# Optimization experiments

Hardware: AMD Instinct MI355X
Metric: run time of the kernel (lower is better)

The kernel has to match this reference:

```python
import jax, jax.numpy as jnp
import numpy as np

N_EMBD = 1024
N_HEAD = 16
HEAD_DIM = N_EMBD // N_HEAD
B, T = 2, 2048
EPS = 1e-5


def _layernorm(x, gamma, beta):
    mu = jnp.mean(x, axis=-1, keepdims=True)
    var = jnp.mean((x - mu) ** 2, axis=-1, keepdims=True)
    return gamma * (x - mu) / jnp.sqrt(var + EPS) + beta


def setup_inputs() -> dict:
    key = jax.random.key(0)
    ks = jax.random.split(key, 12)
    s = 0.02
    d, f = N_EMBD, 4 * N_EMBD
    return {
        "x": jax.random.normal(ks[0], (B, T, d), dtype=jnp.float32),
        "ln1_g": jnp.ones((d,), jnp.float32),
        "ln1_b": jnp.zeros((d,), jnp.float32),
        "wq": jax.random.normal(ks[1], (d, d), jnp.float32) * s,
        "bq": jnp.zeros((d,), jnp.float32),
        "wk": jax.random.normal(ks[2], (d, d), jnp.float32) * s,
        "bk": jnp.zeros((d,), jnp.float32),
        "wv": jax.random.normal(ks[3], (d, d), jnp.float32) * s,
        "bv": jnp.zeros((d,), jnp.float32),
        "wo": jax.random.normal(ks[4], (d, d), jnp.float32) * s,
        "bo": jnp.zeros((d,), jnp.float32),
        "ln2_g": jnp.ones((d,), jnp.float32),
        "ln2_b": jnp.zeros((d,), jnp.float32),
        "w1": jax.random.normal(ks[5], (d, f), jnp.float32) * s,
        "b1": jnp.zeros((f,), jnp.float32),
        "w2": jax.random.normal(ks[6], (f, d), jnp.float32) * s,
        "b2": jnp.zeros((d,), jnp.float32),
    }


def reference(x, ln1_g, ln1_b, wq, bq, wk, bk, wv, bv, wo, bo,
              ln2_g, ln2_b, w1, b1, w2, b2):
    Bn, Tn, C = x.shape
    # --- attention branch (dropout = identity, eval mode) ---
    xn = _layernorm(x, ln1_g, ln1_b)
    q = (xn @ wq + bq).reshape(Bn, Tn, N_HEAD, HEAD_DIM)
    k = (xn @ wk + bk).reshape(Bn, Tn, N_HEAD, HEAD_DIM)
    v = (xn @ wv + bv).reshape(Bn, Tn, N_HEAD, HEAD_DIM)
    scale = 1.0 / jnp.sqrt(jnp.float32(HEAD_DIM))
    scores = jnp.einsum("bqhd,bkhd->bhqk", q, k) * scale  # [B,H,T,T]
    causal = jnp.tril(jnp.ones((Tn, Tn), dtype=bool))
    scores = jnp.where(causal[None, None], scores, -jnp.inf)
    weights = jax.nn.softmax(scores, axis=-1)
    attn = jnp.einsum("bhqk,bkhd->bqhd", weights, v).reshape(Bn, Tn, C)
    x = x + (attn @ wo + bo)
    # --- MLP branch ---
    h = _layernorm(x, ln2_g, ln2_b)
    h = jax.nn.gelu(h @ w1 + b1, approximate=False)
    x = x + (h @ w2 + b2)
    return x
```

## Files before the change

kernel.cpp:

```cpp
#include <hip/hip_runtime.h>
#include <stdint.h>

#define T_SEQ 2048
#define NHEAD 16
#define HDIM 64
#define CDIM 1024
#define FDIM 4096
#define MROWS 4096
#define NQB 32

typedef __bf16 bf16;
typedef __bf16 bf16x8 __attribute__((ext_vector_type(8)));
typedef float f32x4 __attribute__((ext_vector_type(4)));

__device__ __forceinline__ void gload_lds16(const void* g, void* l) {
  __builtin_amdgcn_global_load_lds(
      (const __attribute__((address_space(1))) void*)g,
      (__attribute__((address_space(3))) void*)l, 16, 0, 0);
}

__device__ __forceinline__ void wt_body(const float* __restrict__ src,
                                        bf16* __restrict__ dst, int K, int N,
                                        int k0, int n0) {
  __shared__ float tile[64][65];
  int tid = threadIdx.x;
  int r4 = tid >> 4, c4 = (tid & 15) * 4;
#pragma unroll
  for (int p = 0; p < 4; ++p) {
    int r = p * 16 + r4;
    float4 v = *(const float4*)&src[(size_t)(k0 + r) * N + n0 + c4];
    tile[r][c4] = v.x; tile[r][c4 + 1] = v.y;
    tile[r][c4 + 2] = v.z; tile[r][c4 + 3] = v.w;
  }
  __syncthreads();
  int n8 = tid >> 3, k8 = (tid & 7) * 8;
#pragma unroll
  for (int p = 0; p < 2; ++p) {
    int n = p * 32 + n8;
    union { bf16 h[8]; uint4 u; } t;
#pragma unroll
    for (int j = 0; j < 8; ++j) t.h[j] = (bf16)tile[k8 + j][n];
    *(uint4*)&dst[(size_t)(n0 + n) * K + k0 + k8] = t.u;
  }
}

__global__ void wt_kernel(const float* __restrict__ src, bf16* __restrict__ dst,
                          int K, int N) {
  wt_body(src, dst, K, N, blockIdx.y * 64, blockIdx.x * 64);
}

__global__ void wt4_kernel(const float* s0, const float* s1, const float* s2,
                           const float* s3, bf16* d0, bf16* d1, bf16* d2, bf16* d3) {
  const float* src = blockIdx.z == 0 ? s0 : blockIdx.z == 1 ? s1 : blockIdx.z == 2 ? s2 : s3;
  bf16* dst = blockIdx.z == 0 ? d0 : blockIdx.z == 1 ? d1 : blockIdx.z == 2 ? d2 : d3;
  wt_body(src, dst, 1024, 1024, blockIdx.y * 64, blockIdx.x * 64);
}

__global__ void vt_kernel(const bf16* __restrict__ v, bf16* __restrict__ vt) {
  __shared__ bf16 tile[64][65];
  int bh = blockIdx.y;
  int t0 = blockIdx.x * 64;
  int tid = threadIdx.x;
  const bf16* src = v + (size_t)bh * T_SEQ * HDIM;
  bf16* dst = vt + (size_t)bh * HDIM * T_SEQ;
  int r8 = tid >> 3, c8 = (tid & 7) * 8;
#pragma unroll
  for (int p = 0; p < 2; ++p) {
    int r = p * 32 + r8;
    union { uint4 u; bf16 h[8]; } t;
    t.u = *(const uint4*)&src[(size_t)(t0 + r) * HDIM + c8];
#pragma unroll
    for (int j = 0; j < 8; ++j) tile[r][c8 + j] = t.h[j];
  }
  __syncthreads();
#pragma unroll
  for (int p = 0; p < 2; ++p) {
    int d = p * 32 + r8;
    union { uint4 u; bf16 h[8]; } t;
#pragma unroll
    for (int j = 0; j < 8; ++j) t.h[j] = tile[c8 + j][d];
    *(uint4*)&dst[(size_t)d * T_SEQ + t0 + c8] = t.u;
  }
}

__global__ __launch_bounds__(256)
void ln_kernel(const float* __restrict__ x, const float* __restrict__ g,
               const float* __restrict__ b, bf16* __restrict__ out) {
  int row = blockIdx.x;
  int tid = threadIdx.x;
  float4 v = *(const float4*)&x[(size_t)row * CDIM + tid * 4];
  float s = v.x + v.y + v.z + v.w;
  float ss = v.x * v.x + v.y * v.y + v.z * v.z + v.w * v.w;
#pragma unroll
  for (int off = 1; off < 64; off <<= 1) {
    s += __shfl_xor(s, off, 64);
    ss += __shfl_xor(ss, off, 64);
  }
  __shared__ float red[8];
  int wv = tid >> 6, ln = tid & 63;
  if (ln == 0) { red[wv] = s; red[4 + wv] = ss; }
  __syncthreads();
  s = red[0] + red[1] + red[2] + red[3];
  ss = red[4] + red[5] + red[6] + red[7];
  float mu = s * (1.0f / CDIM);
  float var = ss * (1.0f / CDIM) - mu * mu;
  float rstd = rsqrtf(var + 1e-5f);
  float4 gv = *(const float4*)&g[tid * 4];
  float4 bv = *(const float4*)&b[tid * 4];
  union { bf16 h[4]; uint2 u; } o;
  o.h[0] = (bf16)(gv.x * (v.x - mu) * rstd + bv.x);
  o.h[1] = (bf16)(gv.y * (v.y - mu) * rstd + bv.y);
  o.h[2] = (bf16)(gv.z * (v.z - mu) * rstd + bv.z);
  o.h[3] = (bf16)(gv.w * (v.w - mu) * rstd + bv.w);
  *(uint2*)&out[(size_t)row * CDIM + tid * 4] = o.u;
}

enum { EPI_QKV = 0, EPI_F32RES = 1, EPI_GELU = 2 };

template <int EPI, int TN>
__global__ __launch_bounds__(256, 2)
void gemm_bt(const bf16* __restrict__ A, const bf16* __restrict__ Bt,
             const float* __restrict__ bias, const float* __restrict__ bias2,
             const float* __restrict__ bias3, const float* res,
             void* outp, void* out2, void* out3, int M, int N, int K) {
  constexpr int MR = (TN == 128) ? 4 : 2;
  __shared__ __align__(16) bf16 As[4][128 * 32];
  __shared__ __align__(16) bf16 Bs[4][TN * 32];
  int tid = threadIdx.x;
  int w = tid >> 6, l = tid & 63;
  int lo = l & 15, g = l >> 4;
  int rowb = (TN == 128) ? (w >> 1) * 64 : w * 32;
  int colb = (TN == 128) ? (w & 1) * 64 : 0;

  int nwg = gridDim.x * gridDim.y;
  int orig = blockIdx.y * gridDim.x + blockIdx.x;
  int lid = (orig & 7) * (nwg >> 3) + (orig >> 3);
  int bx = lid % gridDim.x, by = lid / gridDim.x;
  int m0 = by * 128, n0 = bx * TN;

  f32x4 acc[MR][4];
#pragma unroll
  for (int i = 0; i < MR; ++i)
#pragma unroll
    for (int j = 0; j < 4; ++j) acc[i][j] = (f32x4){0.f, 0.f, 0.f, 0.f};

  const bf16* Ab = A + (size_t)m0 * K;
  const bf16* Bb = Bt + (size_t)n0 * K;

  auto STAGE = [&](int t, int buf) {
    int k0 = t * 32;
    int row = (l >> 2);
    int col = ((l & 3) ^ ((l >> 3) & 3)) * 8;
#pragma unroll
    for (int i = 0; i < 2; ++i) {
      int c = w * 2 + i;
      gload_lds16(Ab + (size_t)(c * 16 + row) * K + k0 + col, &As[buf][c * 512]);
    }
    if constexpr (TN == 128) {
#pragma unroll
      for (int i = 0; i < 2; ++i) {
        int c = w * 2 + i;
        gload_lds16(Bb + (size_t)(c * 16 + row) * K + k0 + col, &Bs[buf][c * 512]);
      }
    } else {
      int c = w;
      gload_lds16(Bb + (size_t)(c * 16 + row) * K + k0 + col, &Bs[buf][c * 512]);
    }
  };

  int nt = K >> 5;
  STAGE(0, 0);
  STAGE(1, 1);
  STAGE(2, 2);
  int sw = (lo >> 1) & 3;
  for (int t = 0; t < nt; ++t) {
    if constexpr (TN == 128) {
      if (t + 2 < nt)      asm volatile("s_waitcnt vmcnt(8)" ::: "memory");
      else if (t + 1 < nt) asm volatile("s_waitcnt vmcnt(4)" ::: "memory");
      else                 asm volatile("s_waitcnt vmcnt(0)" ::: "memory");
    } else {
      if (t + 2 < nt)      asm volatile("s_waitcnt vmcnt(6)" ::: "memory");
      else if (t + 1 < nt) asm volatile("s_waitcnt vmcnt(3)" ::: "memory");
      else                 asm volatile("s_waitcnt vmcnt(0)" ::: "memory");
    }
    __builtin_amdgcn_s_barrier();
    __builtin_amdgcn_sched_barrier(0);
    int cur = t & 3;
    bf16x8 af[MR], bfr[4];
#pragma unroll
    for (int m = 0; m < MR; ++m) {
      int R = rowb + m * 16 + lo;
      af[m] = *(const bf16x8*)&As[cur][R * 32 + (g ^ sw) * 8];
    }
#pragma unroll
    for (int n = 0; n < 4; ++n) {
      int R = colb + n * 16 + lo;
      bfr[n] = *(const bf16x8*)&Bs[cur][R * 32 + (g ^ sw) * 8];
    }
    if (t + 3 < nt) STAGE(t + 3, (t + 3) & 3);
    __builtin_amdgcn_s_setprio(1);
#pragma unroll
    for (int m = 0; m < MR; ++m)
#pragma unroll
      for (int n = 0; n < 4; ++n)
        acc[m][n] = __builtin_amdgcn_mfma_f32_16x16x32_bf16(af[m], bfr[n], acc[m][n], 0, 0, 0);
    __builtin_amdgcn_s_setprio(0);
  }

  if constexpr (EPI == EPI_QKV) {
    int which = n0 >> 10;
    const float* bb = which == 0 ? bias : (which == 1 ? bias2 : bias3);
    bf16* ob = (bf16*)(which == 0 ? outp : (which == 1 ? out2 : out3));
#pragma unroll
    for (int m = 0; m < MR; ++m)
#pragma unroll
      for (int n = 0; n < 4; ++n)
#pragma unroll
        for (int j = 0; j < 4; ++j) {
          int row = m0 + rowb + m * 16 + g * 4 + j;
          int col = n0 + colb + n * 16 + lo;
          int cw = col & (CDIM - 1);
          float v = acc[m][n][j] + bb[cw];
          int b = row >> 11, t = row & (T_SEQ - 1);
          int h = cw >> 6, d = cw & (HDIM - 1);
          ob[(((size_t)(b * NHEAD + h)) * T_SEQ + t) * HDIM + d] = (bf16)v;
        }
  } else {
#pragma unroll
    for (int m = 0; m < MR; ++m)
#pragma unroll
      for (int n = 0; n < 4; ++n)
#pragma unroll
        for (int j = 0; j < 4; ++j) {
          int row = m0 + rowb + m * 16 + g * 4 + j;
          int col = n0 + colb + n * 16 + lo;
          float v = acc[m][n][j] + bias[col];
          if constexpr (EPI == EPI_F32RES) {
            ((float*)outp)[(size_t)row * N + col] = v + res[(size_t)row * N + col];
          } else {
            float ge = 0.5f * v * (1.0f + erff(v * 0.70710678118654752f));
            ((bf16*)outp)[(size_t)row * N + col] = (bf16)ge;
          }
        }
  }
}

__device__ __forceinline__ void attn_tile(
    const bf16* __restrict__ Ksb, const bf16* __restrict__ Vsb,
    bf16* __restrict__ Psw, const bf16x8 qf[2], f32x4 Ot[4],
    float& mrun, float& lrun, int lo, int g, int kbase, int myq, bool diag) {
  f32x4 st[4];
#pragma unroll
  for (int kt = 0; kt < 4; ++kt) {
    f32x4 a = (f32x4){0.f, 0.f, 0.f, 0.f};
#pragma unroll
    for (int dh = 0; dh < 2; ++dh) {
      int R = kt * 16 + lo;
      int slot = (dh * 4 + g) ^ (R & 7);
      bf16x8 kf = *(const bf16x8*)&Ksb[R * 64 + slot * 8];
      a = __builtin_amdgcn_mfma_f32_16x16x32_bf16(kf, qf[dh], a, 0, 0, 0);
    }
    st[kt] = a;
  }
  if (diag) {
#pragma unroll
    for (int kt = 0; kt < 4; ++kt)
#pragma unroll
      for (int j = 0; j < 4; ++j) {
        int key = kbase + kt * 16 + g * 4 + j;
        if (key > myq) st[kt][j] = -1e30f;
      }
  }
  float cmax = -1e30f;
#pragma unroll
  for (int kt = 0; kt < 4; ++kt)
#pragma unroll
    for (int j = 0; j < 4; ++j) cmax = fmaxf(cmax, st[kt][j]);
  cmax = fmaxf(cmax, __shfl_xor(cmax, 16, 64));
  cmax = fmaxf(cmax, __shfl_xor(cmax, 32, 64));
  float mnew = fmaxf(mrun, cmax);
  float corr = exp2f(mrun - mnew);
  float csum = 0.f;
#pragma unroll
  for (int kt = 0; kt < 4; ++kt) {
    union { bf16 h[4]; uint2 u; } pk;
#pragma unroll
    for (int j = 0; j < 4; ++j) {
      float pv = exp2f(st[kt][j] - mnew);
      csum += pv;
      pk.h[j] = (bf16)pv;
    }
    *(uint2*)&Psw[lo * 72 + kt * 16 + g * 4] = pk.u;
  }
  csum += __shfl_xor(csum, 16, 64);
  csum += __shfl_xor(csum, 32, 64);
  lrun = lrun * corr + csum;
  mrun = mnew;
#pragma unroll
  for (int dt = 0; dt < 4; ++dt)
#pragma unroll
    for (int j = 0; j < 4; ++j) Ot[dt][j] *= corr;
#pragma unroll
  for (int ks = 0; ks < 2; ++ks) {
    bf16x8 pf = *(const bf16x8*)&Psw[lo * 72 + ks * 32 + g * 8];
#pragma unroll
    for (int dt = 0; dt < 4; ++dt) {
      int R = dt * 16 + lo;
      int slot = (ks * 4 + g) ^ (R & 7);
      bf16x8 vf = *(const bf16x8*)&Vsb[R * 64 + slot * 8];
      Ot[dt] = __builtin_amdgcn_mfma_f32_16x16x32_bf16(vf, pf, Ot[dt], 0, 0, 0);
    }
  }
}

__global__ __launch_bounds__(256, 2)
void attn_kernel(const bf16* __restrict__ q, const bf16* __restrict__ k,
                 const bf16* __restrict__ vt, bf16* __restrict__ out) {
  __shared__ __align__(16) bf16 Ks[2][64 * 64];
  __shared__ __align__(16) bf16 Vs[2][64 * 64];
  __shared__ __align__(16) bf16 Ps[4][16 * 72];
  int tid = threadIdx.x;
  int w = tid >> 6, l = tid & 63;
  int lo = l & 15, g = l >> 4;
  int nwg = gridDim.x * gridDim.y;
  int orig = blockIdx.y * gridDim.x + blockIdx.x;
  int lid = (orig & 7) * (nwg >> 3) + (orig >> 3);
  int p = lid & 15;
  int bh = lid >> 4;
  int qA = p, qB = NQB - 1 - p;
  int nch = qB + 1;
  const bf16* qh = q + (size_t)bh * T_SEQ * HDIM;
  const bf16* kh = k + (size_t)bh * T_SEQ * HDIM;
  const bf16* vh = vt + (size_t)bh * HDIM * T_SEQ;

  const float sc = 0.125f * 1.44269504f;
  bf16x8 qfA[2], qfB[2];
#pragma unroll
  for (int dh = 0; dh < 2; ++dh) {
    bf16x8 tA = *(const bf16x8*)&qh[(size_t)(qA * 64 + w * 16 + lo) * HDIM + dh * 32 + g * 8];
    bf16x8 tB = *(const bf16x8*)&qh[(size_t)(qB * 64 + w * 16 + lo) * HDIM + dh * 32 + g * 8];
#pragma unroll
    for (int j = 0; j < 8; ++j) {
      qfA[dh][j] = (bf16)((float)tA[j] * sc);
      qfB[dh][j] = (bf16)((float)tB[j] * sc);
    }
  }
  int myqA = qA * 64 + w * 16 + lo;
  int myqB = qB * 64 + w * 16 + lo;

  f32x4 OtA[4], OtB[4];
#pragma unroll
  for (int i = 0; i < 4; ++i) {
    OtA[i] = (f32x4){0.f, 0.f, 0.f, 0.f};
    OtB[i] = (f32x4){0.f, 0.f, 0.f, 0.f};
  }
  float mA = -1e30f, lA = 0.f, mB = -1e30f, lB = 0.f;

  int srow8 = l >> 3, s0 = l & 7;
  auto STAGE = [&](int kc, int buf) {
#pragma unroll
    for (int i = 0; i < 2; ++i) {
      int c = w * 2 + i;
      int r = c * 8 + srow8;
      int ecol = (s0 ^ (r & 7)) * 8;
      gload_lds16(&kh[(size_t)(kc * 64 + r) * HDIM + ecol], &Ks[buf][c * 512]);
      gload_lds16(&vh[(size_t)r * T_SEQ + kc * 64 + ecol], &Vs[buf][c * 512]);
    }
  };

  STAGE(0, 0);
  int cur = 0;
  for (int kc = 0; kc < nch; ++kc) {
    __syncthreads();
    if (kc + 1 < nch) STAGE(kc + 1, cur ^ 1);
    attn_tile(Ks[cur], Vs[cur], Ps[w], qfB, OtB, mB, lB, lo, g, kc * 64, myqB,
              kc == nch - 1);
    if (kc <= p)
      attn_tile(Ks[cur], Vs[cur], Ps[w], qfA, OtA, mA, lA, lo, g, kc * 64, myqA,
                kc == p);
    cur ^= 1;
  }

  int b = bh >> 4, h = bh & 15;
  {
    float inv = 1.0f / lA;
    bf16* ob = out + (((size_t)b * T_SEQ + myqA) * NHEAD + h) * HDIM;
#pragma unroll
    for (int dt = 0; dt < 4; ++dt)
#pragma unroll
      for (int j = 0; j < 4; ++j) ob[dt * 16 + g * 4 + j] = (bf16)(OtA[dt][j] * inv);
  }
  {
    float inv = 1.0f / lB;
    bf16* ob = out + (((size_t)b * T_SEQ + myqB) * NHEAD + h) * HDIM;
#pragma unroll
    for (int dt = 0; dt < 4; ++dt)
#pragma unroll
      for (int j = 0; j < 4; ++j) ob[dt * 16 + g * 4 + j] = (bf16)(OtB[dt][j] * inv);
  }
}

extern "C" void kernel_launch(void* const* d_in, const int* in_sizes, int n_in,
                              void* d_out, int out_size, void* d_ws, size_t ws_size,
                              hipStream_t stream) {
  (void)in_sizes; (void)n_in; (void)out_size; (void)ws_size;
  const float* x     = (const float*)d_in[0];
  const float* ln1_g = (const float*)d_in[1];
  const float* ln1_b = (const float*)d_in[2];
  const float* wq    = (const float*)d_in[3];
  const float* bq    = (const float*)d_in[4];
  const float* wk    = (const float*)d_in[5];
  const float* bk    = (const float*)d_in[6];
  const float* wv    = (const float*)d_in[7];
  const float* bv    = (const float*)d_in[8];
  const float* wo    = (const float*)d_in[9];
  const float* bo    = (const float*)d_in[10];
  const float* ln2_g = (const float*)d_in[11];
  const float* ln2_b = (const float*)d_in[12];
  const float* w1    = (const float*)d_in[13];
  const float* b1    = (const float*)d_in[14];
  const float* w2    = (const float*)d_in[15];
  const float* b2    = (const float*)d_in[16];
  float* out = (float*)d_out;

  const size_t MB = 1024ull * 1024ull;
  char* ws = (char*)d_ws;
  bf16* wqkvT = (bf16*)(ws + 0 * MB);
  bf16* wqT = wqkvT;
  bf16* wkT = (bf16*)(ws + 2 * MB);
  bf16* wvT = (bf16*)(ws + 4 * MB);
  bf16* woT = (bf16*)(ws + 6 * MB);
  bf16* w1T = (bf16*)(ws + 8 * MB);
  bf16* w2T = (bf16*)(ws + 16 * MB);
  bf16* xn  = (bf16*)(ws + 24 * MB);
  bf16* qb_ = (bf16*)(ws + 32 * MB);
  bf16* kb_ = (bf16*)(ws + 40 * MB);
  bf16* vb_ = (bf16*)(ws + 48 * MB);
  bf16* vtb = (bf16*)(ws + 56 * MB);
  bf16* aout = (bf16*)(ws + 24 * MB);
  bf16* hn  = (bf16*)(ws + 32 * MB);
  bf16* hb  = (bf16*)(ws + 40 * MB);

  dim3 blk(256);
  wt4_kernel<<<dim3(16, 16, 4), blk, 0, stream>>>(wq, wk, wv, wo, wqT, wkT, wvT, woT);
  wt_kernel<<<dim3(64, 16), blk, 0, stream>>>(w1, w1T, 1024, 4096);
  wt_kernel<<<dim3(16, 64), blk, 0, stream>>>(w2, w2T, 4096, 1024);

  ln_kernel<<<MROWS, blk, 0, stream>>>(x, ln1_g, ln1_b, xn);

  gemm_bt<EPI_QKV, 128><<<dim3(24, 32), blk, 0, stream>>>(
      xn, wqkvT, bq, bk, bv, nullptr, qb_, kb_, vb_, MROWS, 3 * CDIM, CDIM);

  vt_kernel<<<dim3(32, 32), blk, 0, stream>>>(vb_, vtb);
  attn_kernel<<<dim3(16, 32), blk, 0, stream>>>(qb_, kb_, vtb, aout);

  gemm_bt<EPI_F32RES, 64><<<dim3(16, 32), blk, 0, stream>>>(
      aout, woT, bo, nullptr, nullptr, x, out, nullptr, nullptr, MROWS, CDIM, CDIM);

  ln_kernel<<<MROWS, blk, 0, stream>>>(out, ln2_g, ln2_b, hn);

  gemm_bt<EPI_GELU, 128><<<dim3(32, 32), blk, 0, stream>>>(
      hn, w1T, b1, nullptr, nullptr, nullptr, hb, nullptr, nullptr, MROWS, FDIM, CDIM);
  gemm_bt<EPI_F32RES, 64><<<dim3(16, 32), blk, 0, stream>>>(
      hb, w2T, b2, nullptr, nullptr, out, out, nullptr, nullptr, MROWS, CDIM, FDIM);
}
```

Before: 260.2 us.

## Add 256x256-tile 512-thread GEMM for QKV and MLP-up projections

Adds a new GEMM kernel with 256x256 output tiles, 8 waves and a triple-buffered LDS pipeline. The A and B stage loads are split across two half-steps with separate barriers. It is used for the QKV projection (192 blocks) and the first MLP projection (256 blocks), to raise data reuse per block and cut global/LDS traffic. The cost is fewer blocks than the 256 CUs on MI355X, lower occupancy (one block per CU) and high register pressure from 128 accumulators per thread. The old kernel's QKV epilogue is removed since it is no longer used.

Result: faster. 241.4 us (-7.2%).

```diff
diff --git a/kernel.cpp b/kernel.cpp
--- a/kernel.cpp
+++ b/kernel.cpp
@@ -117,6 +117,140 @@
 
 enum { EPI_QKV = 0, EPI_F32RES = 1, EPI_GELU = 2 };
 
+template <int EPI>
+__global__ __launch_bounds__(512, 1)
+void gemm256(const bf16* __restrict__ A, const bf16* __restrict__ Bt,
+             const float* __restrict__ bias, const float* __restrict__ bias2,
+             const float* __restrict__ bias3, const float* res,
+             void* outp, void* out2, void* out3, int M, int N, int K) {
+  __shared__ __align__(16) bf16 As[3][256 * 32];
+  __shared__ __align__(16) bf16 Bs[3][256 * 32];
+  int tid = threadIdx.x;
+  int w = tid >> 6, l = tid & 63;
+  int wr = w >> 2, wc = w & 3;
+  int lo = l & 15, g = l >> 4;
+
+  int nwg = gridDim.x * gridDim.y;
+  int orig = blockIdx.y * gridDim.x + blockIdx.x;
+  int lid = (orig & 7) * (nwg >> 3) + (orig >> 3);
+  int bx = lid % gridDim.x, by = lid / gridDim.x;
+  int m0 = by * 256, n0 = bx * 256;
+
+  f32x4 acc[8][4];
+#pragma unroll
+  for (int i = 0; i < 8; ++i)
+#pragma unroll
+    for (int j = 0; j < 4; ++j) acc[i][j] = (f32x4){0.f, 0.f, 0.f, 0.f};
+
+  const bf16* Ab = A + (size_t)m0 * K;
+  const bf16* Bb = Bt + (size_t)n0 * K;
+
+  int srow = tid >> 2;
+  int scol = ((tid & 3) ^ ((tid >> 3) & 3)) * 8;
+  auto STAGE_A = [&](int t, int buf) {
+    int k0 = t * 32;
+#pragma unroll
+    for (int c = 0; c < 2; ++c)
+      gload_lds16(Ab + (size_t)(c * 128 + srow) * K + k0 + scol,
+                  &As[buf][c * 4096 + w * 512]);
+  };
+  auto STAGE_B = [&](int t, int buf) {
+    int k0 = t * 32;
+#pragma unroll
+    for (int c = 0; c < 2; ++c)
+      gload_lds16(Bb + (size_t)(c * 128 + srow) * K + k0 + scol,
+                  &Bs[buf][c * 4096 + w * 512]);
+  };
+
+  int nt = K >> 5;
+  STAGE_A(0, 0); STAGE_B(0, 0);
+  STAGE_A(1, 1); STAGE_B(1, 1);
+  asm volatile("s_waitcnt vmcnt(4)" ::: "memory");
+  __syncthreads();
+  int sw = (lo >> 1) & 3;
+  int b0 = 0;
+  for (int t = 0; t < nt; ++t) {
+    int b2 = b0 - 1; if (b2 < 0) b2 += 3;
+    bf16x8 af[4], bfr[4];
+#pragma unroll
+    for (int m = 0; m < 4; ++m) {
+      int R = wr * 128 + m * 16 + lo;
+      af[m] = *(const bf16x8*)&As[b0][R * 32 + (g ^ sw) * 8];
+    }
+#pragma unroll
+    for (int n = 0; n < 4; ++n) {
+      int R = wc * 64 + n * 16 + lo;
+      bfr[n] = *(const bf16x8*)&Bs[b0][R * 32 + (g ^ sw) * 8];
+    }
+    if (t + 2 < nt) STAGE_A(t + 2, b2);
+    asm volatile("s_barrier" ::: "memory");
+    __builtin_amdgcn_s_setprio(1);
+#pragma unroll
+    for (int m = 0; m < 4; ++m)
+#pragma unroll
+      for (int n = 0; n < 4; ++n)
+        acc[m][n] = __builtin_amdgcn_mfma_f32_16x16x32_bf16(af[m], bfr[n], acc[m][n], 0, 0, 0);
+    __builtin_amdgcn_s_setprio(0);
+#pragma unroll
+    for (int m = 0; m < 4; ++m) {
+      int R = wr * 128 + (m + 4) * 16 + lo;
+      af[m] = *(const bf16x8*)&As[b0][R * 32 + (g ^ sw) * 8];
+    }
+    if (t + 2 < nt) {
+      STAGE_B(t + 2, b2);
+      asm volatile("s_waitcnt vmcnt(4)" ::: "memory");
+    } else if (t + 1 < nt) {
+      asm volatile("s_waitcnt vmcnt(0)" ::: "memory");
+    }
+    asm volatile("s_barrier" ::: "memory");
+    __builtin_amdgcn_s_setprio(1);
+#pragma unroll
+    for (int m = 0; m < 4; ++m)
+#pragma unroll
+      for (int n = 0; n < 4; ++n)
+        acc[m + 4][n] = __builtin_amdgcn_mfma_f32_16x16x32_bf16(af[m], bfr[n], acc[m + 4][n], 0, 0, 0);
+    __builtin_amdgcn_s_setprio(0);
+    b0 = (b0 == 2) ? 0 : b0 + 1;
+  }
+
+  if constexpr (EPI == EPI_QKV) {
+    int which = n0 >> 10;
+    const float* bb = which == 0 ? bias : (which == 1 ? bias2 : bias3);
+    bf16* ob = (bf16*)(which == 0 ? outp : (which == 1 ? out2 : out3));
+#pragma unroll
+    for (int m = 0; m < 8; ++m)
+#pragma unroll
+      for (int n = 0; n < 4; ++n)
+#pragma unroll
+        for (int j = 0; j < 4; ++j) {
+          int row = m0 + wr * 128 + m * 16 + g * 4 + j;
+          int col = n0 + wc * 64 + n * 16 + lo;
+          int cw = col & (CDIM - 1);
+          float v = acc[m][n][j] + bb[cw];
+          int b = row >> 11, tt = row & (T_SEQ - 1);
+          int h = cw >> 6, d = cw & (HDIM - 1);
+          ob[(((size_t)(b * NHEAD + h)) * T_SEQ + tt) * HDIM + d] = (bf16)v;
+        }
+  } else {
+#pragma unroll
+    for (int m = 0; m < 8; ++m)
+#pragma unroll
+      for (int n = 0; n < 4; ++n)
+#pragma unroll
+        for (int j = 0; j < 4; ++j) {
+          int row = m0 + wr * 128 + m * 16 + g * 4 + j;
+          int col = n0 + wc * 64 + n * 16 + lo;
+          float v = acc[m][n][j] + bias[col];
+          if constexpr (EPI == EPI_F32RES) {
+            ((float*)outp)[(size_t)row * N + col] = v + res[(size_t)row * N + col];
+          } else {
+            float ge = 0.5f * v * (1.0f + erff(v * 0.70710678118654752f));
+            ((bf16*)outp)[(size_t)row * N + col] = (bf16)ge;
+          }
+        }
+  }
+}
+
 template <int EPI, int TN>
 __global__ __launch_bounds__(256, 2)
 void gemm_bt(const bf16* __restrict__ A, const bf16* __restrict__ Bt,
@@ -207,42 +341,22 @@
     __builtin_amdgcn_s_setprio(0);
   }
 
-  if constexpr (EPI == EPI_QKV) {
-    int which = n0 >> 10;
-    const float* bb = which == 0 ? bias : (which == 1 ? bias2 : bias3);
-    bf16* ob = (bf16*)(which == 0 ? outp : (which == 1 ? out2 : out3));
-#pragma unroll
-    for (int m = 0; m < MR; ++m)
-#pragma unroll
-      for (int n = 0; n < 4; ++n)
-#pragma unroll
-        for (int j = 0; j < 4; ++j) {
-          int row = m0 + rowb + m * 16 + g * 4 + j;
-          int col = n0 + colb + n * 16 + lo;
-          int cw = col & (CDIM - 1);
-          float v = acc[m][n][j] + bb[cw];
-          int b = row >> 11, t = row & (T_SEQ - 1);
-          int h = cw >> 6, d = cw & (HDIM - 1);
-          ob[(((size_t)(b * NHEAD + h)) * T_SEQ + t) * HDIM + d] = (bf16)v;
+#pragma unroll
+  for (int m = 0; m < MR; ++m)
+#pragma unroll
+    for (int n = 0; n < 4; ++n)
+#pragma unroll
+      for (int j = 0; j < 4; ++j) {
+        int row = m0 + rowb + m * 16 + g * 4 + j;
+        int col = n0 + colb + n * 16 + lo;
+        float v = acc[m][n][j] + bias[col];
+        if constexpr (EPI == EPI_F32RES) {
+          ((float*)outp)[(size_t)row * N + col] = v + res[(size_t)row * N + col];
+        } else {
+          float ge = 0.5f * v * (1.0f + erff(v * 0.70710678118654752f));
+          ((bf16*)outp)[(size_t)row * N + col] = (bf16)ge;
         }
-  } else {
-#pragma unroll
-    for (int m = 0; m < MR; ++m)
-#pragma unroll
-      for (int n = 0; n < 4; ++n)
-#pragma unroll
-        for (int j = 0; j < 4; ++j) {
-          int row = m0 + rowb + m * 16 + g * 4 + j;
-          int col = n0 + colb + n * 16 + lo;
-          float v = acc[m][n][j] + bias[col];
-          if constexpr (EPI == EPI_F32RES) {
-            ((float*)outp)[(size_t)row * N + col] = v + res[(size_t)row * N + col];
-          } else {
-            float ge = 0.5f * v * (1.0f + erff(v * 0.70710678118654752f));
-            ((bf16*)outp)[(size_t)row * N + col] = (bf16)ge;
-          }
-        }
-  }
+      }
 }
 
 __device__ __forceinline__ void attn_tile(
@@ -448,7 +562,7 @@
 
   ln_kernel<<<MROWS, blk, 0, stream>>>(x, ln1_g, ln1_b, xn);
 
-  gemm_bt<EPI_QKV, 128><<<dim3(24, 32), blk, 0, stream>>>(
+  gemm256<EPI_QKV><<<dim3(12, 16), dim3(512), 0, stream>>>(
       xn, wqkvT, bq, bk, bv, nullptr, qb_, kb_, vb_, MROWS, 3 * CDIM, CDIM);
 
   vt_kernel<<<dim3(32, 32), blk, 0, stream>>>(vb_, vtb);
@@ -459,7 +573,7 @@
 
   ln_kernel<<<MROWS, blk, 0, stream>>>(out, ln2_g, ln2_b, hn);
 
-  gemm_bt<EPI_GELU, 128><<<dim3(32, 32), blk, 0, stream>>>(
+  gemm256<EPI_GELU><<<dim3(16, 16), dim3(512), 0, stream>>>(
       hn, w1T, b1, nullptr, nullptr, nullptr, hb, nullptr, nullptr, MROWS, FDIM, CDIM);
   gemm_bt<EPI_F32RES, 64><<<dim3(16, 32), blk, 0, stream>>>(
       hb, w2T, b2, nullptr, nullptr, out, out, nullptr, nullptr, MROWS, CDIM, FDIM);
```
